# Kernel optimization log

Measured on AMD Instinct MI355X. Metric: run time of the kernel, lower is better.

The kernel has to match this reference:

```python
import jax, jax.numpy as jnp
import numpy as np

M, NN, D, H, DFF, L, EPG = 128, 62, 512, 8, 2048, 4, 600
K1, K2 = 50, 40  # ceil(0.8*62), ceil(0.8*50)
EPS = 1e-5


def _ln(x, g, b):
    mu = x.mean(-1, keepdims=True)
    v = x.var(-1, keepdims=True)
    return (x - mu) * jax.lax.rsqrt(v + EPS) * g + b


def _gcn(x, src, dst, mask, W, b, n):
    # PyG GCNConv: add self-loops, sym-normalized scatter-add aggregation
    h = x @ W
    w = mask.astype(x.dtype)
    deg = 1.0 + jax.ops.segment_sum(w, dst, num_segments=n)  # +1 self-loop
    dis = jax.lax.rsqrt(deg)
    coef = dis[src] * w * dis[dst]
    agg = jax.ops.segment_sum(coef[:, None] * h[src], dst, num_segments=n)
    return agg + h * (dis * dis)[:, None] + b  # second term = self-loop message


def _sagpool(x, src, dst, mask, Ws, bs, m, n_per, k):
    n = m * n_per
    score = _gcn(x, src, dst, mask, Ws, bs, n)[:, 0]
    _, topi = jax.lax.top_k(score.reshape(m, n_per), k)  # per-graph topk
    perm = (topi + jnp.arange(m)[:, None] * n_per).reshape(-1)
    xn = x[perm] * jnp.tanh(score[perm])[:, None]
    # filter_adj: keep edges with both endpoints surviving, remap indices
    nmap = jnp.full((n,), -1, jnp.int32).at[perm].set(jnp.arange(m * k, dtype=jnp.int32))
    ns, nd = nmap[src], nmap[dst]
    keep = mask & (ns >= 0) & (nd >= 0)
    return xn, jnp.where(keep, ns, 0), jnp.where(keep, nd, 0), keep


def _enc_layer(x, Wqkv, bqkv, Wo, bo, W1, b1, W2, b2, g1, be1, g2, be2):
    # post-norm TransformerEncoderLayer, relu activation, eval (no dropout)
    S, B, Dm = x.shape
    dh = Dm // H
    q, k, v = jnp.split(x @ Wqkv + bqkv, 3, axis=-1)
    q = q.reshape(S, B, H, dh)
    k = k.reshape(S, B, H, dh)
    v = v.reshape(S, B, H, dh)
    att = jnp.einsum('sbhd,tbhd->bhst', q, k) * (1.0 / np.sqrt(dh))
    o = jnp.einsum('bhst,tbhd->sbhd', jax.nn.softmax(att, axis=-1), v).reshape(S, B, Dm)
    x = _ln(x + o @ Wo + bo, g1, be1)
    f = jax.nn.relu(x @ W1 + b1) @ W2 + b2
    return _ln(x + f, g2, be2)


def _readout(h, m, k):
    hr = h.reshape(m, k, -1)
    return jnp.concatenate([hr.max(axis=1), hr.mean(axis=1)], axis=-1)  # gmp||gap


def _forward(edge_index, x, bn_g, bn_b, W_emb, enc_Wqkv, enc_bqkv, enc_Wo, enc_bo, enc_W1, enc_b1, enc_W2, enc_b2, enc_g1, enc_be1, enc_g2, enc_be2, W_emb1, conv1_W, conv1_b, convs_W, convs_b, pool1_W, pool1_b, pool2_W, pool2_b, fc1_W, fc1_b, fc2_W, fc2_b, fc3_W, fc3_b):
    m = x.shape[0] // NN
    xr = x.reshape(m, NN, NN)
    # BatchNorm1d(62) in training mode: per-channel stats over (N, L)
    mu = xr.mean(axis=(0, 2), keepdims=True)
    var = xr.var(axis=(0, 2), keepdims=True)
    xb = (xr - mu) * jax.lax.rsqrt(var + EPS) * bn_g[None, :, None] + bn_b[None, :, None]
    t = xb.transpose(1, 0, 2) @ W_emb  # [62, m, D] seq-first
    for l in range(L):
        t = _enc_layer(t, enc_Wqkv[l], enc_bqkv[l], enc_Wo[l], enc_bo[l], enc_W1[l], enc_b1[l], enc_W2[l], enc_b2[l], enc_g1[l], enc_be1[l], enc_g2[l], enc_be2[l])
    # faithful to torch: reshape [62,m,62] directly to [m*62,62] (no permute back)
    xg = (t @ W_emb1).reshape(m * NN, NN)
    src, dst = edge_index[0], edge_index[1]
    mask0 = jnp.ones(src.shape, bool)
    h = jax.nn.relu(_gcn(xg, src, dst, mask0, conv1_W, conv1_b, m * NN))
    h, s1, d1, m1 = _sagpool(h, src, dst, mask0, pool1_W, pool1_b, m, NN, K1)
    x1 = _readout(h, m, K1)
    for l in range(L - 1):
        h = jax.nn.relu(_gcn(h, s1, d1, m1, convs_W[l], convs_b[l], m * K1))
    h, s2, d2, m2 = _sagpool(h, s1, d1, m1, pool2_W, pool2_b, m, K1, K2)
    x2 = _readout(h, m, K2)
    z = x1 + x2
    z = jax.nn.relu(z @ fc1_W + fc1_b)
    z = jax.nn.relu(z @ fc2_W + fc2_b)
    return z @ fc3_W + fc3_b


def setup_inputs():
    key = jax.random.key(0)
    ki = iter(jax.random.split(key, 40))
    def nrm(shape, s=0.05):
        return jax.random.normal(next(ki), shape, jnp.float32) * s
    x = jax.random.normal(next(ki), (M * NN, NN), jnp.float32)
    off = jnp.arange(M, dtype=jnp.int32)[:, None] * NN
    src = jax.random.randint(next(ki), (M, EPG), 0, NN, dtype=jnp.int32) + off
    dst = jax.random.randint(next(ki), (M, EPG), 0, NN, dtype=jnp.int32) + off
    edge_index = jnp.stack([src.reshape(-1), dst.reshape(-1)])
    return dict(
        x=x, edge_index=edge_index,
        bn_g=jnp.ones(NN), bn_b=jnp.zeros(NN),
        W_emb=nrm((NN, D)),
        enc_Wqkv=nrm((L, D, 3 * D)), enc_bqkv=jnp.zeros((L, 3 * D)),
        enc_Wo=nrm((L, D, D)), enc_bo=jnp.zeros((L, D)),
        enc_W1=nrm((L, D, DFF)), enc_b1=jnp.zeros((L, DFF)),
        enc_W2=nrm((L, DFF, D)), enc_b2=jnp.zeros((L, D)),
        enc_g1=jnp.ones((L, D)), enc_be1=jnp.zeros((L, D)),
        enc_g2=jnp.ones((L, D)), enc_be2=jnp.zeros((L, D)),
        W_emb1=nrm((D, NN)),
        conv1_W=nrm((NN, D)), conv1_b=jnp.zeros(D),
        convs_W=nrm((L - 1, D, D)), convs_b=jnp.zeros((L - 1, D)),
        pool1_W=nrm((D, 1)), pool1_b=jnp.zeros(1),
        pool2_W=nrm((D, 1)), pool2_b=jnp.zeros(1),
        fc1_W=nrm((2 * D, D)), fc1_b=jnp.zeros(D),
        fc2_W=nrm((D, D // 2)), fc2_b=jnp.zeros(D // 2),
        fc3_W=nrm((D // 2, 2)), fc3_b=jnp.zeros(2))


def reference(x, edge_index, bn_g, bn_b, W_emb, enc_Wqkv, enc_bqkv, enc_Wo, enc_bo, enc_W1, enc_b1, enc_W2, enc_b2, enc_g1, enc_be1, enc_g2, enc_be2, W_emb1, conv1_W, conv1_b, convs_W, convs_b, pool1_W, pool1_b, pool2_W, pool2_b, fc1_W, fc1_b, fc2_W, fc2_b, fc3_W, fc3_b):
    return _forward(edge_index, x, bn_g, bn_b, W_emb, enc_Wqkv, enc_bqkv, enc_Wo, enc_bo, enc_W1, enc_b1, enc_W2, enc_b2, enc_g1, enc_be1, enc_g2, enc_be2, W_emb1, conv1_W, conv1_b, convs_W, convs_b, pool1_W, pool1_b, pool2_W, pool2_b, fc1_W, fc1_b, fc2_W, fc2_b, fc3_W, fc3_b)
```

## Files before the change

kernel.cpp:

```cpp
#include <hip/hip_runtime.h>
#include <float.h>
#include <math.h>

#define MG 128
#define NNODE 62
#define DD 512
#define NH 8
#define DH 64
#define DFF 2048
#define NLAYER 4
#define EPG 600
#define KP1 50
#define KP2 40
#define NTOK (MG*NNODE)
#define NEDGE (MG*EPG)
#define EPSV 1e-5f
#define PW 68

typedef unsigned short u16;
using bf16x8 = __attribute__((ext_vector_type(8))) short;
using f32x4  = __attribute__((ext_vector_type(4))) float;

__device__ __forceinline__ float wave_sum(float v) {
  for (int off = 32; off; off >>= 1) v += __shfl_xor(v, off);
  return v;
}
__device__ __forceinline__ float wave_max(float v) {
  for (int off = 32; off; off >>= 1) v = fmaxf(v, __shfl_xor(v, off));
  return v;
}
__device__ __forceinline__ u16 f2b(float x) {
  union { float f; unsigned u; } v; v.f = x;
  unsigned r = v.u + 0x7fffu + ((v.u >> 16) & 1u);
  return (u16)(r >> 16);
}
__device__ __forceinline__ float b2f(u16 h) {
  union { float f; unsigned u; } v; v.u = ((unsigned)h) << 16;
  return v.f;
}
__device__ __forceinline__ void f2bsplit(float x, u16& h, u16& l) {
  h = f2b(x);
  l = f2b(x - b2f(h));
}
__device__ __forceinline__ void load_lds16(const u16* g, u16* l) {
  __builtin_amdgcn_global_load_lds(
      (const __attribute__((address_space(1))) unsigned int*)(const void*)g,
      (__attribute__((address_space(3))) unsigned int*)(void*)l, 16, 0, 0);
}
__device__ __forceinline__ void cvt8(const float* __restrict__ p, bf16x8& vh, bf16x8& vl) {
  #pragma unroll
  for (int e = 0; e < 8; ++e) {
    u16 h, l; f2bsplit(p[e], h, l);
    vh[e] = (short)h; vl[e] = (short)l;
  }
}
__device__ __forceinline__ void cvt8s(const float* __restrict__ p, bf16x8& vh, bf16x8& vl) {
  #pragma unroll
  for (int e = 0; e < 8; ++e) {
    u16 h, l; f2bsplit(p[e*PW], h, l);
    vh[e] = (short)h; vl[e] = (short)l;
  }
}

__global__ __launch_bounds__(256) void bn_stats_kernel(const float* __restrict__ x,
    float* __restrict__ mu, float* __restrict__ rs) {
  int s = blockIdx.x;
  float sum = 0.f, sq = 0.f;
  for (int i = threadIdx.x; i < MG*NNODE; i += 256) {
    int b = i / NNODE, j = i - b*NNODE;
    float v = x[(size_t)(b*NNODE + s)*NNODE + j];
    sum += v; sq += v*v;
  }
  __shared__ float r1[4], r2[4];
  sum = wave_sum(sum); sq = wave_sum(sq);
  int wv = threadIdx.x >> 6, lane = threadIdx.x & 63;
  if (lane == 0) { r1[wv] = sum; r2[wv] = sq; }
  __syncthreads();
  if (threadIdx.x == 0) {
    float S = r1[0]+r1[1]+r1[2]+r1[3];
    float Q = r2[0]+r2[1]+r2[2]+r2[3];
    float m = S / (float)(MG*NNODE);
    float var = Q / (float)(MG*NNODE) - m*m;
    mu[s] = m;
    rs[s] = rsqrtf(var + EPSV);
  }
}

__global__ __launch_bounds__(256) void embed_kernel(const float* __restrict__ x,
    const float* __restrict__ mu, const float* __restrict__ rs,
    const float* __restrict__ gg, const float* __restrict__ bb,
    const float* __restrict__ W, float* __restrict__ T,
    u16* __restrict__ Th, u16* __restrict__ Tl) {
  int tok = blockIdx.x;
  int s = tok >> 7, b = tok & 127;
  __shared__ float xb[NNODE];
  if (threadIdx.x < NNODE) {
    float v = x[(size_t)(b*NNODE + s)*NNODE + threadIdx.x];
    xb[threadIdx.x] = (v - mu[s]) * rs[s] * gg[s] + bb[s];
  }
  __syncthreads();
  int d = threadIdx.x;
  float a0 = 0.f, a1 = 0.f;
  for (int j = 0; j < NNODE; ++j) {
    float xv = xb[j];
    a0 += xv * W[(size_t)j*DD + d];
    a1 += xv * W[(size_t)j*DD + d + 256];
  }
  size_t o = (size_t)tok*DD + d;
  T[o] = a0; T[o+256] = a1;
  u16 h, l;
  f2bsplit(a0, h, l); Th[o] = h; Tl[o] = l;
  f2bsplit(a1, h, l); Th[o+256] = h; Tl[o+256] = l;
}

__global__ __launch_bounds__(256) void gemm_kernel(const float* __restrict__ A,
    const float* __restrict__ B, float* __restrict__ C, int M, int N, int K) {
  __shared__ float As[16][68];
  __shared__ float Bs[16][68];
  int bm = blockIdx.y * 64, bn = blockIdx.x * 64;
  int tid = threadIdx.x;
  int tx = tid & 15, ty = tid >> 4;
  float acc[4][4] = {};
  for (int k0 = 0; k0 < K; k0 += 16) {
    {
      int row = tid >> 2; int kk = (tid & 3) * 4;
      int gm = bm + row;
      #pragma unroll
      for (int i = 0; i < 4; ++i) {
        int gk = k0 + kk + i;
        As[kk+i][row] = (gm < M && gk < K) ? A[(size_t)gm*K + gk] : 0.f;
      }
    }
    {
      int krow = tid >> 4; int nn = (tid & 15) * 4;
      int gk = k0 + krow;
      #pragma unroll
      for (int i = 0; i < 4; ++i) {
        int gn = bn + nn + i;
        Bs[krow][nn+i] = (gk < K && gn < N) ? B[(size_t)gk*N + gn] : 0.f;
      }
    }
    __syncthreads();
    #pragma unroll
    for (int k = 0; k < 16; ++k) {
      float a[4], bb2[4];
      #pragma unroll
      for (int i = 0; i < 4; ++i) a[i] = As[k][ty*4+i];
      #pragma unroll
      for (int j = 0; j < 4; ++j) bb2[j] = Bs[k][tx*4+j];
      #pragma unroll
      for (int i = 0; i < 4; ++i)
        #pragma unroll
        for (int j = 0; j < 4; ++j) acc[i][j] += a[i]*bb2[j];
    }
    __syncthreads();
  }
  #pragma unroll
  for (int i = 0; i < 4; ++i) {
    int gm = bm + ty*4 + i;
    if (gm >= M) continue;
    #pragma unroll
    for (int j = 0; j < 4; ++j) {
      int gn = bn + tx*4 + j;
      if (gn >= N) continue;
      C[(size_t)gm*N + gn] = acc[i][j];
    }
  }
}

__device__ __forceinline__ void transpose_split_tile(const float* __restrict__ W,
    u16* __restrict__ th, u16* __restrict__ tl,
    int K, int N, int Kp, int bx, int by, float (*t)[65]) {
  int k0 = by*64, n0 = bx*64;
  for (int i = threadIdx.x; i < 64*64; i += 256) {
    int r = i >> 6, c = i & 63;
    int gk = k0 + r, gn = n0 + c;
    t[r][c] = (gk < K && gn < N) ? W[(size_t)gk*N + gn] : 0.f;
  }
  __syncthreads();
  for (int i = threadIdx.x; i < 64*64; i += 256) {
    int r = i >> 6, c = i & 63;
    int gn = n0 + r, gk = k0 + c;
    u16 h, l; f2bsplit(t[c][r], h, l);
    th[(size_t)gn*Kp + gk] = h;
    tl[(size_t)gn*Kp + gk] = l;
  }
}

__global__ __launch_bounds__(256) void layerT_kernel(
    const float* __restrict__ Wqkv, const float* __restrict__ Wo,
    const float* __restrict__ W1, const float* __restrict__ W2,
    u16* WQh, u16* WQl, u16* WOh, u16* WOl,
    u16* W1h, u16* W1l, u16* W2h, u16* W2l) {
  __shared__ float t[64][65];
  int b = blockIdx.x;
  if (b < 192)      transpose_split_tile(Wqkv, WQh, WQl, 512, 1536, 512, b % 24, b / 24, t);
  else if (b < 256) { int q = b - 192; transpose_split_tile(Wo, WOh, WOl, 512, 512, 512, q % 8, q / 8, t); }
  else if (b < 512) { int q = b - 256; transpose_split_tile(W1, W1h, W1l, 512, 2048, 512, q % 32, q / 32, t); }
  else              { int q = b - 512; transpose_split_tile(W2, W2h, W2l, 2048, 512, 2048, q % 8, q / 8, t); }
}

__global__ __launch_bounds__(256) void gcnT_kernel(
    const float* __restrict__ WC, const float* __restrict__ convs_W,
    u16* CTh, u16* CTl, u16* CVh, u16* CVl) {
  __shared__ float t[64][65];
  int job = blockIdx.x >> 6, q = blockIdx.x & 63;
  int bx = q % 8, by = q / 8;
  if (job == 0) transpose_split_tile(WC, CTh, CTl, 512, 512, 512, bx, by, t);
  else {
    int l = job - 1;
    transpose_split_tile(convs_W + (size_t)l*DD*DD,
        CVh + (size_t)l*DD*DD, CVl + (size_t)l*DD*DD, 512, 512, 512, bx, by, t);
  }
}

template<bool RELU, int OUTMODE>
__global__ __launch_bounds__(256) void gemm3_kernel(
    const u16* __restrict__ Ah, const u16* __restrict__ Al,
    const u16* __restrict__ Bh, const u16* __restrict__ Bl,
    const float* __restrict__ bias,
    float* __restrict__ Cf, u16* __restrict__ Ch, u16* __restrict__ Cl,
    int Nreal, int Nstride, int Kp, int KC) {
  __shared__ alignas(16) u16 sA[2][2][4096];
  __shared__ alignas(16) u16 sB[2][2][4096];
  unsigned nx = gridDim.x, ny = gridDim.y;
  unsigned nwg = nx * ny * gridDim.z;
  unsigned lb = blockIdx.x + nx*(blockIdx.y + ny*blockIdx.z);
  unsigned swz = lb;
  if ((nwg & 7u) == 0u) {
    unsigned cpx = nwg >> 3;
    swz = (lb & 7u)*cpx + (lb >> 3);
  }
  unsigned bxi = swz % nx;
  unsigned rem = swz / nx;
  unsigned byi = rem % ny;
  unsigned bzi = rem / ny;
  int bm = byi * 128, bn = bxi * 128;
  int z = bzi;
  int tid = threadIdx.x;
  int wv = tid >> 6, lane = tid & 63;
  int wr = (wv >> 1) * 64, wc = (wv & 1) * 64;
  f32x4 acc[4][4];
  #pragma unroll
  for (int i = 0; i < 4; ++i)
    #pragma unroll
    for (int j = 0; j < 4; ++j) acc[i][j] = (f32x4){0.f,0.f,0.f,0.f};

  int r0 = tid >> 2;
  int lin = (tid & 3) * 8;
  int c0 = lin ^ (((r0 >> 1) & 3) << 3);
  int r1 = r0 + 64;
  int c1 = lin ^ (((r1 >> 1) & 3) << 3);
  int fr = lane & 15, fo = (lane >> 4) * 8;

  auto stage = [&](int k0, int bi) {
    size_t a0 = (size_t)(bm + r0)*Kp + k0 + c0;
    size_t a1 = (size_t)(bm + r1)*Kp + k0 + c1;
    size_t b0 = (size_t)(bn + r0)*Kp + k0 + c0;
    size_t b1 = (size_t)(bn + r1)*Kp + k0 + c1;
    load_lds16(Ah + a0, &sA[bi][0][tid*8]);
    load_lds16(Ah + a1, &sA[bi][0][2048 + tid*8]);
    load_lds16(Al + a0, &sA[bi][1][tid*8]);
    load_lds16(Al + a1, &sA[bi][1][2048 + tid*8]);
    load_lds16(Bh + b0, &sB[bi][0][tid*8]);
    load_lds16(Bh + b1, &sB[bi][0][2048 + tid*8]);
    load_lds16(Bl + b0, &sB[bi][1][tid*8]);
    load_lds16(Bl + b1, &sB[bi][1][2048 + tid*8]);
  };

  int kbeg = z * KC;
  int nk = KC >> 5;
  stage(kbeg, 0);
  int cur = 0;
  for (int t = 0; t < nk; ++t) {
    if (t + 1 < nk) {
      stage(kbeg + (t+1)*32, cur ^ 1);
      asm volatile("s_waitcnt vmcnt(8)" ::: "memory");
    } else {
      asm volatile("s_waitcnt vmcnt(0)" ::: "memory");
    }
    __builtin_amdgcn_s_barrier();
    __builtin_amdgcn_sched_barrier(0);
    bf16x8 ah[4], al[4], bh[4], bl[4];
    #pragma unroll
    for (int i = 0; i < 4; ++i) {
      int ra = wr + i*16 + fr;
      int ea = ra*32 + (fo ^ (((ra >> 1) & 3) << 3));
      ah[i] = *(const bf16x8*)&sA[cur][0][ea];
      al[i] = *(const bf16x8*)&sA[cur][1][ea];
      int rb = wc + i*16 + fr;
      int eb = rb*32 + (fo ^ (((rb >> 1) & 3) << 3));
      bh[i] = *(const bf16x8*)&sB[cur][0][eb];
      bl[i] = *(const bf16x8*)&sB[cur][1][eb];
    }
    #pragma unroll
    for (int i = 0; i < 4; ++i)
      #pragma unroll
      for (int j = 0; j < 4; ++j) {
        acc[i][j] = __builtin_amdgcn_mfma_f32_16x16x32_bf16(ah[i], bh[j], acc[i][j], 0, 0, 0);
        acc[i][j] = __builtin_amdgcn_mfma_f32_16x16x32_bf16(ah[i], bl[j], acc[i][j], 0, 0, 0);
        acc[i][j] = __builtin_amdgcn_mfma_f32_16x16x32_bf16(al[i], bh[j], acc[i][j], 0, 0, 0);
      }
    __builtin_amdgcn_s_barrier();
    cur ^= 1;
  }
  size_t pstride = (size_t)gridDim.y * 128 * Nstride;
  int cr = (lane >> 4) * 4, cc = lane & 15;
  #pragma unroll
  for (int i = 0; i < 4; ++i) {
    #pragma unroll
    for (int j = 0; j < 4; ++j) {
      int gn = bn + wc + j*16 + cc;
      if (gn >= Nstride) continue;
      #pragma unroll
      for (int q = 0; q < 4; ++q) {
        int gm = bm + wr + i*16 + cr + q;
        float v = acc[i][j][q];
        if (gn < Nreal) { if (bias && z == 0) v += bias[gn]; } else v = 0.f;
        if (RELU) v = fmaxf(v, 0.f);
        if (OUTMODE == 0) {
          Cf[(size_t)z*pstride + (size_t)gm*Nstride + gn] = v;
        } else if (OUTMODE == 1) {
          size_t o = (size_t)z*pstride + (size_t)gm*Nstride + gn;
          u16 h, l; f2bsplit(v, h, l);
          Ch[o] = h; Cl[o] = l;
        } else {
          int which = gn >> 9, hh2 = (gn >> 6) & 7, d = gn & 63;
          int b2 = gm & 127, s2 = gm >> 7;
          Cf[(size_t)((which*NH + hh2)*MG + b2)*4096 + s2*64 + d] = v;
        }
      }
    }
  }
}

__global__ __launch_bounds__(256) void attn_kernel(const float* __restrict__ QKV,
    u16* __restrict__ Oh, u16* __restrict__ Ol) {
  int b = blockIdx.x >> 3, h = blockIdx.x & 7;
  __shared__ float sQ[64*PW];
  __shared__ float sK[64*PW];
  __shared__ float sV[64*PW];
  u16* sPh = (u16*)sK;
  u16* sPl = ((u16*)sK) + 4096;
  float* Ss = sQ;
  int tid = threadIdx.x, wv = tid >> 6, lane = tid & 63;
  int fr = lane & 15, fq = lane >> 4;
  size_t base0 = (size_t)(h*MG + b)*4096;
  const float* Qg = QKV + base0;
  const float* Kg = QKV + (size_t)NH*MG*4096 + base0;
  const float* Vg = QKV + (size_t)2*NH*MG*4096 + base0;
  #pragma unroll
  for (int i = 0; i < 4; ++i) {
    int c = tid + i*256;
    int r = c >> 4, col = (c & 15) * 4;
    f32x4 q4 = *(const f32x4*)(Qg + (size_t)c*4);
    f32x4 k4 = *(const f32x4*)(Kg + (size_t)c*4);
    f32x4 v4 = *(const f32x4*)(Vg + (size_t)c*4);
    *(f32x4*)&sQ[r*PW + col] = q4;
    *(f32x4*)&sK[r*PW + col] = k4;
    *(f32x4*)&sV[r*PW + col] = v4;
  }
  if (tid < 128) sV[(62 + (tid >> 6))*PW + (tid & 63)] = 0.f;
  __syncthreads();
  int rA = 16*wv + fr;
  bf16x8 qh[2], ql[2];
  #pragma unroll
  for (int kk = 0; kk < 2; ++kk)
    cvt8(&sQ[rA*PW + 32*kk + 8*fq], qh[kk], ql[kk]);
  __syncthreads();
  f32x4 accS[4];
  #pragma unroll
  for (int j = 0; j < 4; ++j) accS[j] = (f32x4){0.f,0.f,0.f,0.f};
  __builtin_amdgcn_s_setprio(1);
  #pragma unroll
  for (int kk = 0; kk < 2; ++kk) {
    #pragma unroll
    for (int j = 0; j < 4; ++j) {
      int rB = 16*j + fr;
      bf16x8 kh, kl;
      cvt8(&sK[rB*PW + 32*kk + 8*fq], kh, kl);
      accS[j] = __builtin_amdgcn_mfma_f32_16x16x32_bf16(qh[kk], kh, accS[j], 0, 0, 0);
      accS[j] = __builtin_amdgcn_mfma_f32_16x16x32_bf16(qh[kk], kl, accS[j], 0, 0, 0);
      accS[j] = __builtin_amdgcn_mfma_f32_16x16x32_bf16(ql[kk], kh, accS[j], 0, 0, 0);
    }
  }
  __builtin_amdgcn_s_setprio(0);
  #pragma unroll
  for (int j = 0; j < 4; ++j)
    #pragma unroll
    for (int q = 0; q < 4; ++q)
      Ss[(16*wv + fq*4 + q)*PW + 16*j + fr] = accS[j][q];
  __syncthreads();
  for (int rr = 0; rr < 16; ++rr) {
    int row = 16*wv + rr;
    float sv = (lane < NNODE) ? Ss[row*PW + lane]*0.125f : -FLT_MAX;
    float mx = wave_max(sv);
    float e = (lane < NNODE) ? expf(sv - mx) : 0.f;
    float sm = wave_sum(e);
    float p = e / sm;
    u16 ph, pl; f2bsplit(p, ph, pl);
    int pos = row*64 + ((((lane >> 3) ^ (row & 7)) << 3) | (lane & 7));
    sPh[pos] = ph; sPl[pos] = pl;
  }
  __syncthreads();
  f32x4 accO[4];
  #pragma unroll
  for (int j = 0; j < 4; ++j) accO[j] = (f32x4){0.f,0.f,0.f,0.f};
  __builtin_amdgcn_s_setprio(1);
  #pragma unroll
  for (int kk = 0; kk < 2; ++kk) {
    int cha = (((4*kk + fq) ^ (rA & 7)) << 3);
    bf16x8 pah = *(const bf16x8*)&sPh[rA*64 + cha];
    bf16x8 pal = *(const bf16x8*)&sPl[rA*64 + cha];
    #pragma unroll
    for (int j = 0; j < 4; ++j) {
      bf16x8 vh, vl;
      cvt8s(&sV[(32*kk + 8*fq)*PW + 16*j + fr], vh, vl);
      accO[j] = __builtin_amdgcn_mfma_f32_16x16x32_bf16(pah, vh, accO[j], 0, 0, 0);
      accO[j] = __builtin_amdgcn_mfma_f32_16x16x32_bf16(pah, vl, accO[j], 0, 0, 0);
      accO[j] = __builtin_amdgcn_mfma_f32_16x16x32_bf16(pal, vh, accO[j], 0, 0, 0);
    }
  }
  __builtin_amdgcn_s_setprio(0);
  #pragma unroll
  for (int j = 0; j < 4; ++j) {
    #pragma unroll
    for (int q = 0; q < 4; ++q) {
      int s2 = 16*wv + fq*4 + q;
      if (s2 < NNODE) {
        int d = 16*j + fr;
        size_t o = ((size_t)(s2*MG + b))*DD + h*DH + d;
        u16 hh2, ll2; f2bsplit(accO[j][q], hh2, ll2);
        Oh[o] = hh2; Ol[o] = ll2;
      }
    }
  }
}

__global__ __launch_bounds__(256) void add_ln_kernel(float* __restrict__ X,
    const float* __restrict__ P, int nchunk,
    const float* __restrict__ gg, const float* __restrict__ bb,
    u16* __restrict__ Xh, u16* __restrict__ Xl) {
  size_t row = blockIdx.x;
  int t = threadIdx.x;
  const size_t MN = (size_t)NTOK*DD;
  float r0 = 0.f, r1 = 0.f;
  for (int z = 0; z < nchunk; ++z) {
    r0 += P[z*MN + row*DD + t];
    r1 += P[z*MN + row*DD + t + 256];
  }
  float v0 = X[row*DD + t] + r0;
  float v1 = X[row*DD + t + 256] + r1;
  __shared__ float red[4];
  float s = wave_sum(v0 + v1);
  int wv = t >> 6, lane = t & 63;
  if (lane == 0) red[wv] = s;
  __syncthreads();
  float mu = (red[0]+red[1]+red[2]+red[3]) * (1.f/DD);
  float d0 = v0 - mu, d1 = v1 - mu;
  float q = wave_sum(d0*d0 + d1*d1);
  __syncthreads();
  if (lane == 0) red[wv] = q;
  __syncthreads();
  float var = (red[0]+red[1]+red[2]+red[3]) * (1.f/DD);
  float rs = rsqrtf(var + EPSV);
  float o0 = d0*rs*gg[t] + bb[t];
  float o1 = d1*rs*gg[t+256] + bb[t+256];
  X[row*DD + t] = o0;
  X[row*DD + t+256] = o1;
  u16 h, l;
  f2bsplit(o0, h, l); Xh[row*DD + t] = h; Xl[row*DD + t] = l;
  f2bsplit(o1, h, l); Xh[row*DD + t+256] = h; Xl[row*DD + t+256] = l;
}

__global__ void fill_int_kernel(int* p, int v, int n) {
  int i = blockIdx.x*256 + threadIdx.x;
  if (i < n) p[i] = v;
}
__global__ void zero_f_kernel(float* p, int n) {
  int i = blockIdx.x*256 + threadIdx.x;
  if (i < n) p[i] = 0.f;
}
__global__ void count_deg_kernel(const int* __restrict__ dst, int* deg, int n) {
  int e = blockIdx.x*256 + threadIdx.x;
  if (e < n) atomicAdd(&deg[dst[e]], 1);
}
__global__ void dis_kernel(const int* __restrict__ deg, float* dis, int n) {
  int i = blockIdx.x*256+threadIdx.x;
  if (i < n) dis[i] = rsqrtf((float)deg[i]);
}
__global__ void coef0_kernel(const int* __restrict__ src, const int* __restrict__ dst,
                             const float* __restrict__ dis, float* coef) {
  int e = blockIdx.x*256+threadIdx.x;
  if (e < NEDGE) coef[e] = dis[src[e]]*dis[dst[e]];
}
__global__ void coef1_kernel(const int* __restrict__ src, const int* __restrict__ dst,
                             const int* __restrict__ keep,
                             const float* __restrict__ dis, float* coef) {
  int e = blockIdx.x*256+threadIdx.x;
  if (e < NEDGE) coef[e] = keep[e] ? dis[src[e]]*dis[dst[e]] : 0.f;
}

__global__ __launch_bounds__(64) void diagA_kernel(const float* __restrict__ dis,
    float* __restrict__ AG, int NP) {
  int g = blockIdx.x, lane = threadIdx.x;
  if (lane < NP) {
    float d = dis[g*NP + lane];
    AG[(size_t)g*4096 + lane*64 + lane] = d*d;
  }
}
__global__ __launch_bounds__(256) void edgeA_kernel(const int* __restrict__ src,
    const int* __restrict__ dst, const float* __restrict__ coef,
    float* __restrict__ AG, int NP) {
  int e = blockIdx.x*256 + threadIdx.x;
  if (e >= NEDGE) return;
  float c = coef[e];
  if (c == 0.f) return;
  int g = e / EPG;
  int ls = src[e] - g*NP, ld = dst[e] - g*NP;
  atomicAdd(&AG[(size_t)g*4096 + ld*64 + ls], c);
}

__global__ __launch_bounds__(256) void dense_agg_kernel(
    const float* __restrict__ AG,
    const float* __restrict__ P, int nchunk, size_t mn,
    const float* __restrict__ bias,
    float* __restrict__ Hout, int NP, int relu,
    u16* __restrict__ outh, u16* __restrict__ outl) {
  int g = blockIdx.x >> 3;
  int ct = (blockIdx.x & 7) * 64;
  __shared__ float hls[64*64];
  __shared__ float At[64*68];
  int base = g * NP;
  for (int idx = threadIdx.x; idx < 64*64; idx += 256) {
    int r = idx >> 6, c = idx & 63;
    float v = 0.f;
    if (r < NP) {
      for (int z = 0; z < nchunk; ++z)
        v += P[z*mn + (size_t)(base+r)*DD + ct + c];
    }
    hls[idx] = v;
    At[c*68 + r] = AG[(size_t)g*4096 + idx];
  }
  __syncthreads();
  int wv = threadIdx.x >> 6, lane = threadIdx.x & 63;
  int i0 = wv * 16;
  f32x4 acc[4];
  #pragma unroll
  for (int q = 0; q < 4; ++q) acc[q] = (f32x4){0.f,0.f,0.f,0.f};
  for (int j = 0; j < NP; ++j) {
    float hv = hls[j*64 + lane];
    const f32x4* ap = (const f32x4*)&At[j*68 + i0];
    f32x4 a0 = ap[0], a1 = ap[1], a2 = ap[2], a3 = ap[3];
    #pragma unroll
    for (int t = 0; t < 4; ++t) {
      acc[0][t] += a0[t] * hv;
      acc[1][t] += a1[t] * hv;
      acc[2][t] += a2[t] * hv;
      acc[3][t] += a3[t] * hv;
    }
  }
  float bv = bias[ct + lane];
  #pragma unroll
  for (int q = 0; q < 4; ++q) {
    #pragma unroll
    for (int t = 0; t < 4; ++t) {
      int i = i0 + q*4 + t;
      if (i < NP) {
        float v = acc[q][t] + bv;
        if (relu) v = fmaxf(v, 0.f);
        size_t o = (size_t)(base+i)*DD + ct + lane;
        Hout[o] = v;
        if (outh) { u16 h, l; f2bsplit(v, h, l); outh[o] = h; outl[o] = l; }
      }
    }
  }
}

__global__ __launch_bounds__(64) void dense_score_kernel(
    const float* __restrict__ AG, const float* __restrict__ hsv,
    const float* __restrict__ pb, float* __restrict__ sc, int NP) {
  int g = blockIdx.x, lane = threadIdx.x;
  __shared__ float hls[64];
  __shared__ float At[64*65];
  hls[lane] = (lane < NP) ? hsv[g*NP + lane] : 0.f;
  for (int idx = lane; idx < 64*64; idx += 64) {
    int i = idx >> 6, j = idx & 63;
    At[j*65 + i] = AG[(size_t)g*4096 + idx];
  }
  __syncthreads();
  if (lane < NP) {
    float acc = 0.f;
    for (int j = 0; j < NP; ++j) acc += At[j*65 + lane] * hls[j];
    sc[g*NP + lane] = acc + pb[0];
  }
}

__global__ __launch_bounds__(256) void gemv_kernel(const float* __restrict__ h,
    const float* __restrict__ wv, float* __restrict__ out, int n) {
  int node = blockIdx.x*4 + (threadIdx.x >> 6);
  int lane = threadIdx.x & 63;
  if (node >= n) return;
  const float* row = h + (size_t)node*DD;
  float acc = 0.f;
  for (int d = lane; d < DD; d += 64) acc += row[d]*wv[d];
  acc = wave_sum(acc);
  if (lane == 0) out[node] = acc;
}

__global__ __launch_bounds__(64) void topk_kernel(const float* __restrict__ sc,
    int* __restrict__ perm, int NP, int KK) {
  int g = blockIdx.x, lane = threadIdx.x;
  float v = (lane < NP) ? sc[g*NP+lane] : -FLT_MAX;
  for (int r = 0; r < KK; ++r) {
    float bv = v; int bi = lane;
    for (int off = 32; off; off >>= 1) {
      float ov = __shfl_xor(bv, off);
      int oi = __shfl_xor(bi, off);
      if (ov > bv || (ov == bv && oi < bi)) { bv = ov; bi = oi; }
    }
    if (lane == 0) perm[g*KK + r] = bi;
    if (lane == bi) v = -FLT_MAX;
  }
}

__global__ __launch_bounds__(256) void gather_kernel(const float* __restrict__ h,
    const float* __restrict__ sc, const int* __restrict__ perm,
    float* __restrict__ xn, u16* __restrict__ outh, u16* __restrict__ outl,
    int NP, int KK) {
  int j = blockIdx.x;
  int g = j / KK;
  int pi = perm[j];
  float t = tanhf(sc[g*NP + pi]);
  const float* srow = h + (size_t)(g*NP + pi)*DD;
  size_t o = (size_t)j*DD + threadIdx.x;
  float v0 = srow[threadIdx.x]*t;
  float v1 = srow[threadIdx.x+256]*t;
  xn[o] = v0; xn[o+256] = v1;
  if (outh) {
    u16 hh, ll;
    f2bsplit(v0, hh, ll); outh[o] = hh; outl[o] = ll;
    f2bsplit(v1, hh, ll); outh[o+256] = hh; outl[o+256] = ll;
  }
}

__global__ void nmap_scatter_kernel(const int* __restrict__ perm, int* __restrict__ nmap) {
  int j = blockIdx.x*256 + threadIdx.x;
  if (j < MG*KP1) nmap[(j/KP1)*NNODE + perm[j]] = j;
}

__global__ void filter_kernel(const int* __restrict__ src0, const int* __restrict__ dst0,
    const int* __restrict__ nmap, int* __restrict__ es, int* __restrict__ ed,
    int* __restrict__ keep, int* __restrict__ deg1) {
  int e = blockIdx.x*256+threadIdx.x;
  if (e >= NEDGE) return;
  int ns = nmap[src0[e]], nd = nmap[dst0[e]];
  int k = (ns >= 0) && (nd >= 0);
  es[e] = k ? ns : 0;
  ed[e] = k ? nd : 0;
  keep[e] = k;
  if (k) atomicAdd(&deg1[nd], 1);
}

__global__ __launch_bounds__(256) void readout_kernel(const float* __restrict__ h,
    float* __restrict__ z, int KK, int acc) {
  int g = blockIdx.x;
  for (int c = threadIdx.x; c < DD; c += 256) {
    float mx = -FLT_MAX, sm = 0.f;
    for (int r = 0; r < KK; ++r) {
      float v = h[(size_t)(g*KK+r)*DD + c];
      mx = fmaxf(mx, v); sm += v;
    }
    float mean = sm / (float)KK;
    if (acc) { z[(size_t)g*1024 + c] += mx; z[(size_t)g*1024 + 512 + c] += mean; }
    else     { z[(size_t)g*1024 + c]  = mx; z[(size_t)g*1024 + 512 + c]  = mean; }
  }
}

__global__ __launch_bounds__(256) void mlp1_kernel(const float* __restrict__ Z,
    const float* __restrict__ W1, float* __restrict__ Pm) {
  int b = blockIdx.x;
  int g = b >> 2, zc = b & 3;
  __shared__ float z[256];
  int t = threadIdx.x;
  z[t] = Z[(size_t)g*1024 + zc*256 + t];
  __syncthreads();
  const float* Wb = W1 + (size_t)zc*256*512;
  float a0 = 0.f, a1 = 0.f;
  for (int k = 0; k < 256; ++k) {
    float zv = z[k];
    a0 += zv * Wb[(size_t)k*512 + t];
    a1 += zv * Wb[(size_t)k*512 + t + 256];
  }
  size_t o = ((size_t)zc*MG + g)*512;
  Pm[o + t] = a0;
  Pm[o + t + 256] = a1;
}

__global__ __launch_bounds__(256) void mlp2_kernel(const float* __restrict__ Pm,
    const float* __restrict__ b1,
    const float* __restrict__ W2, const float* __restrict__ b2,
    const float* __restrict__ W3, const float* __restrict__ b3,
    float* __restrict__ out) {
  int g = blockIdx.x;
  int t = threadIdx.x;
  int wv = t >> 6, lane = t & 63;
  __shared__ float h1[512];
  __shared__ float p2[4][256];
  __shared__ float h2[256];
  #pragma unroll
  for (int half = 0; half < 2; ++half) {
    int n = t + half*256;
    float a = b1[n];
    #pragma unroll
    for (int zc = 0; zc < 4; ++zc) a += Pm[((size_t)zc*MG + g)*512 + n];
    h1[n] = fmaxf(a, 0.f);
  }
  __syncthreads();
  {
    float a[4] = {0.f, 0.f, 0.f, 0.f};
    for (int k = wv*128; k < wv*128 + 128; ++k) {
      float hv = h1[k];
      #pragma unroll
      for (int q = 0; q < 4; ++q)
        a[q] += hv * W2[(size_t)k*256 + lane + q*64];
    }
    #pragma unroll
    for (int q = 0; q < 4; ++q) p2[wv][lane + q*64] = a[q];
  }
  __syncthreads();
  h2[t] = fmaxf(p2[0][t] + p2[1][t] + p2[2][t] + p2[3][t] + b2[t], 0.f);
  __syncthreads();
  if (wv < 2) {
    float acc = 0.f;
    for (int k = lane; k < 256; k += 64) acc += h2[k]*W3[(size_t)k*2 + wv];
    acc = wave_sum(acc);
    if (lane == 0) out[(size_t)g*2 + wv] = acc + b3[wv];
  }
}

extern "C" void kernel_launch(void* const* d_in, const int* in_sizes, int n_in,
                              void* d_out, int out_size, void* d_ws, size_t ws_size,
                              hipStream_t stream) {
  const float* x       = (const float*)d_in[0];
  const int*   edge    = (const int*)d_in[1];
  const float* bn_g    = (const float*)d_in[2];
  const float* bn_b    = (const float*)d_in[3];
  const float* W_emb   = (const float*)d_in[4];
  const float* Wqkv    = (const float*)d_in[5];
  const float* bqkv    = (const float*)d_in[6];
  const float* Wo      = (const float*)d_in[7];
  const float* bo      = (const float*)d_in[8];
  const float* W1      = (const float*)d_in[9];
  const float* b1      = (const float*)d_in[10];
  const float* W2      = (const float*)d_in[11];
  const float* b2      = (const float*)d_in[12];
  const float* g1      = (const float*)d_in[13];
  const float* be1     = (const float*)d_in[14];
  const float* g2      = (const float*)d_in[15];
  const float* be2     = (const float*)d_in[16];
  const float* W_emb1  = (const float*)d_in[17];
  const float* conv1_W = (const float*)d_in[18];
  const float* conv1_b = (const float*)d_in[19];
  const float* convs_W = (const float*)d_in[20];
  const float* convs_b = (const float*)d_in[21];
  const float* pool1_W = (const float*)d_in[22];
  const float* pool1_b = (const float*)d_in[23];
  const float* pool2_W = (const float*)d_in[24];
  const float* pool2_b = (const float*)d_in[25];
  const float* fc1_W   = (const float*)d_in[26];
  const float* fc1_b   = (const float*)d_in[27];
  const float* fc2_W   = (const float*)d_in[28];
  const float* fc2_b   = (const float*)d_in[29];
  const float* fc3_W   = (const float*)d_in[30];
  const float* fc3_b   = (const float*)d_in[31];
  (void)in_sizes; (void)n_in; (void)out_size; (void)ws_size;

  const int* srcp = edge;
  const int* dstp = edge + NEDGE;

  char* wsb = (char*)d_ws;
  size_t off = 0;
  auto alloc = [&](size_t bytes)->void* {
    void* p = wsb + off;
    off += (bytes + 255) & ~(size_t)255;
    return p;
  };
  const size_t MN = (size_t)NTOK*DD;
  float* T    = (float*)alloc(MN*4);
  size_t qkvB = (size_t)3*NH*MG*4096*4, ffnB = (size_t)NTOK*DFF*2*2;
  char* BIGU  = (char*)alloc(qkvB > ffnB ? qkvB : ffnB);
  u16* BIGh   = (u16*)BIGU;
  u16* BIGl   = BIGh + (size_t)NTOK*DFF;
  float* QKVf = (float*)BIGU;
  float* PART = (float*)alloc(4*MN*4);
  u16* Th   = (u16*)alloc(MN*2);
  u16* Tl   = (u16*)alloc(MN*2);
  u16* ATh  = (u16*)alloc(MN*2);
  u16* ATl  = (u16*)alloc(MN*2);
  u16* Hh   = (u16*)alloc((size_t)MG*KP1*DD*2);
  u16* Hl   = (u16*)alloc((size_t)MG*KP1*DD*2);
  u16* WQh  = (u16*)alloc((size_t)1536*512*2);
  u16* WQl  = (u16*)alloc((size_t)1536*512*2);
  u16* WOh  = (u16*)alloc((size_t)512*512*2);
  u16* WOl  = (u16*)alloc((size_t)512*512*2);
  u16* W1h  = (u16*)alloc((size_t)2048*512*2);
  u16* W1l  = (u16*)alloc((size_t)2048*512*2);
  u16* W2h  = (u16*)alloc((size_t)512*2048*2);
  u16* W2l  = (u16*)alloc((size_t)512*2048*2);
  float* WCf = (float*)alloc((size_t)512*512*4);
  u16* CTh  = (u16*)alloc((size_t)512*512*2);
  u16* CTl  = (u16*)alloc((size_t)512*512*2);
  u16* CVh  = (u16*)alloc((size_t)3*512*512*2);
  u16* CVl  = (u16*)alloc((size_t)3*512*512*2);
  float* AG0 = (float*)alloc((size_t)MG*4096*4);
  float* AG1 = (float*)alloc((size_t)MG*4096*4);
  float* MU   = (float*)alloc(NNODE*4);
  float* RS   = (float*)alloc(NNODE*4);
  int*   DEG0 = (int*)alloc(NTOK*4);
  float* DIS0 = (float*)alloc(NTOK*4);
  float* COEF0= (float*)alloc(NEDGE*4);
  float* HS   = (float*)alloc(NTOK*4);
  float* SC   = (float*)alloc(NTOK*4);
  int*   PERM1= (int*)alloc(MG*KP1*4);
  int*   NMAP = (int*)alloc(NTOK*4);
  int*   ES1  = (int*)alloc(NEDGE*4);
  int*   ED1  = (int*)alloc(NEDGE*4);
  int*   KEEP1= (int*)alloc(NEDGE*4);
  int*   DEG1 = (int*)alloc(MG*KP1*4);
  float* DIS1 = (float*)alloc(MG*KP1*4);
  float* COEF1= (float*)alloc(NEDGE*4);
  int*   PERM2= (int*)alloc(MG*KP2*4);
  float* Z    = (float*)alloc(MG*1024*4);
  float* Pm   = (float*)alloc((size_t)4*MG*512*4);

  float* PA = PART;
  float* PB = PART + 2*MN;

  bn_stats_kernel<<<NNODE, 256, 0, stream>>>(x, MU, RS);
  embed_kernel<<<NTOK, 256, 0, stream>>>(x, MU, RS, bn_g, bn_b, W_emb, T, Th, Tl);
  fill_int_kernel<<<(NTOK+255)/256, 256, 0, stream>>>(DEG0, 1, NTOK);
  count_deg_kernel<<<(NEDGE+255)/256, 256, 0, stream>>>(dstp, DEG0, NEDGE);
  dis_kernel<<<(NTOK+255)/256, 256, 0, stream>>>(DEG0, DIS0, NTOK);
  coef0_kernel<<<(NEDGE+255)/256, 256, 0, stream>>>(srcp, dstp, DIS0, COEF0);
  zero_f_kernel<<<(MG*4096+255)/256, 256, 0, stream>>>(AG0, MG*4096);
  diagA_kernel<<<MG, 64, 0, stream>>>(DIS0, AG0, NNODE);
  edgeA_kernel<<<(NEDGE+255)/256, 256, 0, stream>>>(srcp, dstp, COEF0, AG0, NNODE);
  gemm_kernel<<<dim3(8,8), 256, 0, stream>>>(W_emb1, conv1_W, WCf, 512, 512, NNODE);
  gcnT_kernel<<<256, 256, 0, stream>>>(WCf, convs_W, CTh, CTl, CVh, CVl);

  for (int l = 0; l < NLAYER; ++l) {
    layerT_kernel<<<768, 256, 0, stream>>>(
        Wqkv + (size_t)l*DD*3*DD, Wo + (size_t)l*DD*DD,
        W1 + (size_t)l*DD*DFF, W2 + (size_t)l*DFF*DD,
        WQh, WQl, WOh, WOl, W1h, W1l, W2h, W2l);
    gemm3_kernel<false,2><<<dim3(12,62,1), 256, 0, stream>>>(Th, Tl, WQh, WQl,
        bqkv + (size_t)l*3*DD, QKVf, nullptr, nullptr, 3*DD, 3*DD, DD, DD);
    attn_kernel<<<MG*NH, 256, 0, stream>>>(QKVf, ATh, ATl);
    gemm3_kernel<false,0><<<dim3(4,62,2), 256, 0, stream>>>(ATh, ATl, WOh, WOl,
        bo + (size_t)l*DD, PART, nullptr, nullptr, DD, DD, DD, 256);
    add_ln_kernel<<<NTOK, 256, 0, stream>>>(T, PART, 2,
        g1 + (size_t)l*DD, be1 + (size_t)l*DD, Th, Tl);
    gemm3_kernel<true,1><<<dim3(16,62,1), 256, 0, stream>>>(Th, Tl, W1h, W1l,
        b1 + (size_t)l*DFF, nullptr, BIGh, BIGl, DFF, DFF, DD, DD);
    gemm3_kernel<false,0><<<dim3(4,62,2), 256, 0, stream>>>(BIGh, BIGl, W2h, W2l,
        b2 + (size_t)l*DD, PART, nullptr, nullptr, DD, DD, DFF, 1024);
    add_ln_kernel<<<NTOK, 256, 0, stream>>>(T, PART, 2,
        g2 + (size_t)l*DD, be2 + (size_t)l*DD, Th, Tl);
  }

  gemm3_kernel<false,0><<<dim3(4,62,2), 256, 0, stream>>>(Th, Tl, CTh, CTl,
      nullptr, PA, nullptr, nullptr, DD, DD, DD, 256);
  dense_agg_kernel<<<MG*8, 256, 0, stream>>>(AG0, PA, 2, MN, conv1_b,
      PA, NNODE, 1, nullptr, nullptr);

  gemv_kernel<<<(NTOK+3)/4, 256, 0, stream>>>(PA, pool1_W, HS, NTOK);
  dense_score_kernel<<<MG, 64, 0, stream>>>(AG0, HS, pool1_b, SC, NNODE);
  topk_kernel<<<MG, 64, 0, stream>>>(SC, PERM1, NNODE, KP1);
  gather_kernel<<<MG*KP1, 256, 0, stream>>>(PA, SC, PERM1, PA + MN, Hh, Hl, NNODE, KP1);
  readout_kernel<<<MG, 256, 0, stream>>>(PA + MN, Z, KP1, 0);

  fill_int_kernel<<<(NTOK+255)/256, 256, 0, stream>>>(NMAP, -1, NTOK);
  nmap_scatter_kernel<<<(MG*KP1+255)/256, 256, 0, stream>>>(PERM1, NMAP);
  fill_int_kernel<<<(MG*KP1+255)/256, 256, 0, stream>>>(DEG1, 1, MG*KP1);
  filter_kernel<<<(NEDGE+255)/256, 256, 0, stream>>>(srcp, dstp, NMAP, ES1, ED1, KEEP1, DEG1);
  dis_kernel<<<(MG*KP1+255)/256, 256, 0, stream>>>(DEG1, DIS1, MG*KP1);
  coef1_kernel<<<(NEDGE+255)/256, 256, 0, stream>>>(ES1, ED1, KEEP1, DIS1, COEF1);
  zero_f_kernel<<<(MG*4096+255)/256, 256, 0, stream>>>(AG1, MG*4096);
  diagA_kernel<<<MG, 64, 0, stream>>>(DIS1, AG1, KP1);
  edgeA_kernel<<<(NEDGE+255)/256, 256, 0, stream>>>(ES1, ED1, COEF1, AG1, KP1);

  const size_t MNP = (size_t)MG*KP1*DD;
  float* bases[3] = { PB, PA, PB };
  float* hfin = nullptr;
  for (int l = 0; l < NLAYER-1; ++l) {
    float* Pb = bases[l];
    gemm3_kernel<false,0><<<dim3(4,50,2), 256, 0, stream>>>(Hh, Hl, CVh + (size_t)l*DD*DD,
        CVl + (size_t)l*DD*DD, nullptr, Pb, nullptr, nullptr, DD, DD, DD, 256);
    dense_agg_kernel<<<MG*8, 256, 0, stream>>>(AG1, Pb, 2, MNP, convs_b + (size_t)l*DD,
        Pb, KP1, 1, (l < NLAYER-2) ? Hh : nullptr, (l < NLAYER-2) ? Hl : nullptr);
    hfin = Pb;
  }

  gemv_kernel<<<(MG*KP1+3)/4, 256, 0, stream>>>(hfin, pool2_W, HS, MG*KP1);
  dense_score_kernel<<<MG, 64, 0, stream>>>(AG1, HS, pool2_b, SC, KP1);
  topk_kernel<<<MG, 64, 0, stream>>>(SC, PERM2, KP1, KP2);
  gather_kernel<<<MG*KP2, 256, 0, stream>>>(hfin, SC, PERM2, PA, nullptr, nullptr, KP1, KP2);
  readout_kernel<<<MG, 256, 0, stream>>>(PA, Z, KP2, 1);

  mlp1_kernel<<<MG*4, 256, 0, stream>>>(Z, fc1_W, Pm);
  mlp2_kernel<<<MG, 256, 0, stream>>>(Pm, fc1_b, fc2_W, fc2_b, fc3_W, fc3_b, (float*)d_out);
}
```

Baseline: 1.642 ms.

## Batch weight transposes, drop fp32 residual copy, hoist GEMM stage pointers

```diff
diff --git a/kernel.cpp b/kernel.cpp
--- a/kernel.cpp
+++ b/kernel.cpp
@@ -89,7 +89,7 @@
 __global__ __launch_bounds__(256) void embed_kernel(const float* __restrict__ x,
     const float* __restrict__ mu, const float* __restrict__ rs,
     const float* __restrict__ gg, const float* __restrict__ bb,
-    const float* __restrict__ W, float* __restrict__ T,
+    const float* __restrict__ W,
     u16* __restrict__ Th, u16* __restrict__ Tl) {
   int tok = blockIdx.x;
   int s = tok >> 7, b = tok & 127;
@@ -107,7 +107,6 @@
     a1 += xv * W[(size_t)j*DD + d + 256];
   }
   size_t o = (size_t)tok*DD + d;
-  T[o] = a0; T[o+256] = a1;
   u16 h, l;
   f2bsplit(a0, h, l); Th[o] = h; Tl[o] = l;
   f2bsplit(a1, h, l); Th[o+256] = h; Tl[o+256] = l;
@@ -187,17 +186,24 @@
   }
 }
 
-__global__ __launch_bounds__(256) void layerT_kernel(
+__global__ __launch_bounds__(256) void allT_kernel(
     const float* __restrict__ Wqkv, const float* __restrict__ Wo,
     const float* __restrict__ W1, const float* __restrict__ W2,
     u16* WQh, u16* WQl, u16* WOh, u16* WOl,
     u16* W1h, u16* W1l, u16* W2h, u16* W2l) {
   __shared__ float t[64][65];
-  int b = blockIdx.x;
-  if (b < 192)      transpose_split_tile(Wqkv, WQh, WQl, 512, 1536, 512, b % 24, b / 24, t);
-  else if (b < 256) { int q = b - 192; transpose_split_tile(Wo, WOh, WOl, 512, 512, 512, q % 8, q / 8, t); }
-  else if (b < 512) { int q = b - 256; transpose_split_tile(W1, W1h, W1l, 512, 2048, 512, q % 32, q / 32, t); }
-  else              { int q = b - 512; transpose_split_tile(W2, W2h, W2l, 2048, 512, 2048, q % 8, q / 8, t); }
+  int layer = blockIdx.x / 768;
+  int b = blockIdx.x % 768;
+  const float* wqkv = Wqkv + (size_t)layer*DD*3*DD;
+  const float* wo   = Wo   + (size_t)layer*DD*DD;
+  const float* w1   = W1   + (size_t)layer*DD*DFF;
+  const float* w2   = W2   + (size_t)layer*DFF*DD;
+  size_t oq = (size_t)layer*1536*512, oo = (size_t)layer*512*512;
+  size_t o1 = (size_t)layer*2048*512, o2 = (size_t)layer*512*2048;
+  if (b < 192)      transpose_split_tile(wqkv, WQh+oq, WQl+oq, 512, 1536, 512, b % 24, b / 24, t);
+  else if (b < 256) { int q = b - 192; transpose_split_tile(wo, WOh+oo, WOl+oo, 512, 512, 512, q % 8, q / 8, t); }
+  else if (b < 512) { int q = b - 256; transpose_split_tile(w1, W1h+o1, W1l+o1, 512, 2048, 512, q % 32, q / 32, t); }
+  else              { int q = b - 512; transpose_split_tile(w2, W2h+o2, W2l+o2, 2048, 512, 2048, q % 8, q / 8, t); }
 }
 
 __global__ __launch_bounds__(256) void gcnT_kernel(
@@ -253,28 +259,32 @@
   int c1 = lin ^ (((r1 >> 1) & 3) << 3);
   int fr = lane & 15, fo = (lane >> 4) * 8;
 
-  auto stage = [&](int k0, int bi) {
-    size_t a0 = (size_t)(bm + r0)*Kp + k0 + c0;
-    size_t a1 = (size_t)(bm + r1)*Kp + k0 + c1;
-    size_t b0 = (size_t)(bn + r0)*Kp + k0 + c0;
-    size_t b1 = (size_t)(bn + r1)*Kp + k0 + c1;
-    load_lds16(Ah + a0, &sA[bi][0][tid*8]);
-    load_lds16(Ah + a1, &sA[bi][0][2048 + tid*8]);
-    load_lds16(Al + a0, &sA[bi][1][tid*8]);
-    load_lds16(Al + a1, &sA[bi][1][2048 + tid*8]);
-    load_lds16(Bh + b0, &sB[bi][0][tid*8]);
-    load_lds16(Bh + b1, &sB[bi][0][2048 + tid*8]);
-    load_lds16(Bl + b0, &sB[bi][1][tid*8]);
-    load_lds16(Bl + b1, &sB[bi][1][2048 + tid*8]);
+  int kbeg = z * KC;
+  const u16* pA0 = Ah + (size_t)(bm + r0)*Kp + kbeg + c0;
+  const u16* pA1 = Ah + (size_t)(bm + r1)*Kp + kbeg + c1;
+  const u16* pB0 = Bh + (size_t)(bn + r0)*Kp + kbeg + c0;
+  const u16* pB1 = Bh + (size_t)(bn + r1)*Kp + kbeg + c1;
+  const ptrdiff_t dA = Al - Ah;
+  const ptrdiff_t dB = Bl - Bh;
+
+  auto stage = [&](int bi) {
+    load_lds16(pA0,      &sA[bi][0][tid*8]);
+    load_lds16(pA1,      &sA[bi][0][2048 + tid*8]);
+    load_lds16(pA0 + dA, &sA[bi][1][tid*8]);
+    load_lds16(pA1 + dA, &sA[bi][1][2048 + tid*8]);
+    load_lds16(pB0,      &sB[bi][0][tid*8]);
+    load_lds16(pB1,      &sB[bi][0][2048 + tid*8]);
+    load_lds16(pB0 + dB, &sB[bi][1][tid*8]);
+    load_lds16(pB1 + dB, &sB[bi][1][2048 + tid*8]);
+    pA0 += 32; pA1 += 32; pB0 += 32; pB1 += 32;
   };
 
-  int kbeg = z * KC;
   int nk = KC >> 5;
-  stage(kbeg, 0);
+  stage(0);
   int cur = 0;
   for (int t = 0; t < nk; ++t) {
     if (t + 1 < nk) {
-      stage(kbeg + (t+1)*32, cur ^ 1);
+      stage(cur ^ 1);
       asm volatile("s_waitcnt vmcnt(8)" ::: "memory");
     } else {
       asm volatile("s_waitcnt vmcnt(0)" ::: "memory");
@@ -437,10 +447,10 @@
   }
 }
 
-__global__ __launch_bounds__(256) void add_ln_kernel(float* __restrict__ X,
+__global__ __launch_bounds__(256) void add_ln_kernel(
+    u16* __restrict__ Xh, u16* __restrict__ Xl,
     const float* __restrict__ P, int nchunk,
-    const float* __restrict__ gg, const float* __restrict__ bb,
-    u16* __restrict__ Xh, u16* __restrict__ Xl) {
+    const float* __restrict__ gg, const float* __restrict__ bb) {
   size_t row = blockIdx.x;
   int t = threadIdx.x;
   const size_t MN = (size_t)NTOK*DD;
@@ -449,8 +459,8 @@
     r0 += P[z*MN + row*DD + t];
     r1 += P[z*MN + row*DD + t + 256];
   }
-  float v0 = X[row*DD + t] + r0;
-  float v1 = X[row*DD + t + 256] + r1;
+  float v0 = b2f(Xh[row*DD + t]) + b2f(Xl[row*DD + t]) + r0;
+  float v1 = b2f(Xh[row*DD + t + 256]) + b2f(Xl[row*DD + t + 256]) + r1;
   __shared__ float red[4];
   float s = wave_sum(v0 + v1);
   int wv = t >> 6, lane = t & 63;
@@ -466,8 +476,6 @@
   float rs = rsqrtf(var + EPSV);
   float o0 = d0*rs*gg[t] + bb[t];
   float o1 = d1*rs*gg[t+256] + bb[t+256];
-  X[row*DD + t] = o0;
-  X[row*DD + t+256] = o1;
   u16 h, l;
   f2bsplit(o0, h, l); Xh[row*DD + t] = h; Xl[row*DD + t] = l;
   f2bsplit(o1, h, l); Xh[row*DD + t+256] = h; Xl[row*DD + t+256] = l;
@@ -787,7 +795,6 @@
     return p;
   };
   const size_t MN = (size_t)NTOK*DD;
-  float* T    = (float*)alloc(MN*4);
   size_t qkvB = (size_t)3*NH*MG*4096*4, ffnB = (size_t)NTOK*DFF*2*2;
   char* BIGU  = (char*)alloc(qkvB > ffnB ? qkvB : ffnB);
   u16* BIGh   = (u16*)BIGU;
@@ -800,14 +807,14 @@
   u16* ATl  = (u16*)alloc(MN*2);
   u16* Hh   = (u16*)alloc((size_t)MG*KP1*DD*2);
   u16* Hl   = (u16*)alloc((size_t)MG*KP1*DD*2);
-  u16* WQh  = (u16*)alloc((size_t)1536*512*2);
-  u16* WQl  = (u16*)alloc((size_t)1536*512*2);
-  u16* WOh  = (u16*)alloc((size_t)512*512*2);
-  u16* WOl  = (u16*)alloc((size_t)512*512*2);
-  u16* W1h  = (u16*)alloc((size_t)2048*512*2);
-  u16* W1l  = (u16*)alloc((size_t)2048*512*2);
-  u16* W2h  = (u16*)alloc((size_t)512*2048*2);
-  u16* W2l  = (u16*)alloc((size_t)512*2048*2);
+  u16* WQh  = (u16*)alloc((size_t)4*1536*512*2);
+  u16* WQl  = (u16*)alloc((size_t)4*1536*512*2);
+  u16* WOh  = (u16*)alloc((size_t)4*512*512*2);
+  u16* WOl  = (u16*)alloc((size_t)4*512*512*2);
+  u16* W1h  = (u16*)alloc((size_t)4*2048*512*2);
+  u16* W1l  = (u16*)alloc((size_t)4*2048*512*2);
+  u16* W2h  = (u16*)alloc((size_t)4*512*2048*2);
+  u16* W2l  = (u16*)alloc((size_t)4*512*2048*2);
   float* WCf = (float*)alloc((size_t)512*512*4);
   u16* CTh  = (u16*)alloc((size_t)512*512*2);
   u16* CTl  = (u16*)alloc((size_t)512*512*2);
@@ -838,7 +845,9 @@
   float* PB = PART + 2*MN;
 
   bn_stats_kernel<<<NNODE, 256, 0, stream>>>(x, MU, RS);
-  embed_kernel<<<NTOK, 256, 0, stream>>>(x, MU, RS, bn_g, bn_b, W_emb, T, Th, Tl);
+  embed_kernel<<<NTOK, 256, 0, stream>>>(x, MU, RS, bn_g, bn_b, W_emb, Th, Tl);
+  allT_kernel<<<4*768, 256, 0, stream>>>(Wqkv, Wo, W1, W2,
+      WQh, WQl, WOh, WOl, W1h, W1l, W2h, W2l);
   fill_int_kernel<<<(NTOK+255)/256, 256, 0, stream>>>(DEG0, 1, NTOK);
   count_deg_kernel<<<(NEDGE+255)/256, 256, 0, stream>>>(dstp, DEG0, NEDGE);
   dis_kernel<<<(NTOK+255)/256, 256, 0, stream>>>(DEG0, DIS0, NTOK);
@@ -850,23 +859,21 @@
   gcnT_kernel<<<256, 256, 0, stream>>>(WCf, convs_W, CTh, CTl, CVh, CVl);
 
   for (int l = 0; l < NLAYER; ++l) {
-    layerT_kernel<<<768, 256, 0, stream>>>(
-        Wqkv + (size_t)l*DD*3*DD, Wo + (size_t)l*DD*DD,
-        W1 + (size_t)l*DD*DFF, W2 + (size_t)l*DFF*DD,
-        WQh, WQl, WOh, WOl, W1h, W1l, W2h, W2l);
-    gemm3_kernel<false,2><<<dim3(12,62,1), 256, 0, stream>>>(Th, Tl, WQh, WQl,
+    size_t oq = (size_t)l*1536*512, oo = (size_t)l*512*512;
+    size_t o1 = (size_t)l*2048*512, o2 = (size_t)l*512*2048;
+    gemm3_kernel<false,2><<<dim3(12,62,1), 256, 0, stream>>>(Th, Tl, WQh+oq, WQl+oq,
         bqkv + (size_t)l*3*DD, QKVf, nullptr, nullptr, 3*DD, 3*DD, DD, DD);
     attn_kernel<<<MG*NH, 256, 0, stream>>>(QKVf, ATh, ATl);
-    gemm3_kernel<false,0><<<dim3(4,62,2), 256, 0, stream>>>(ATh, ATl, WOh, WOl,
+    gemm3_kernel<false,0><<<dim3(4,62,2), 256, 0, stream>>>(ATh, ATl, WOh+oo, WOl+oo,
         bo + (size_t)l*DD, PART, nullptr, nullptr, DD, DD, DD, 256);
-    add_ln_kernel<<<NTOK, 256, 0, stream>>>(T, PART, 2,
-        g1 + (size_t)l*DD, be1 + (size_t)l*DD, Th, Tl);
-    gemm3_kernel<true,1><<<dim3(16,62,1), 256, 0, stream>>>(Th, Tl, W1h, W1l,
+    add_ln_kernel<<<NTOK, 256, 0, stream>>>(Th, Tl, PART, 2,
+        g1 + (size_t)l*DD, be1 + (size_t)l*DD);
+    gemm3_kernel<true,1><<<dim3(16,62,1), 256, 0, stream>>>(Th, Tl, W1h+o1, W1l+o1,
         b1 + (size_t)l*DFF, nullptr, BIGh, BIGl, DFF, DFF, DD, DD);
-    gemm3_kernel<false,0><<<dim3(4,62,2), 256, 0, stream>>>(BIGh, BIGl, W2h, W2l,
+    gemm3_kernel<false,0><<<dim3(4,62,2), 256, 0, stream>>>(BIGh, BIGl, W2h+o2, W2l+o2,
         b2 + (size_t)l*DD, PART, nullptr, nullptr, DD, DD, DFF, 1024);
-    add_ln_kernel<<<NTOK, 256, 0, stream>>>(T, PART, 2,
-        g2 + (size_t)l*DD, be2 + (size_t)l*DD, Th, Tl);
+    add_ln_kernel<<<NTOK, 256, 0, stream>>>(Th, Tl, PART, 2,
+        g2 + (size_t)l*DD, be2 + (size_t)l*DD);
   }
 
   gemm3_kernel<false,0><<<dim3(4,62,2), 256, 0, stream>>>(Th, Tl, CTh, CTl,
```

Result: no change. 1.618 ms, median of 3 (-1.5%).
